# Performance work log

Measured on AMD Instinct MI355X. Metric: run time of the kernel, lower is better.

## Reference

```python
import jax, jax.numpy as jnp
import numpy as np

B, D, N = 2, 256, 8192   # batch, in_channels, sequence length
CI = 128                 # inter_channels
BN_EPS = 1e-5


def conv1x1(w, b, x):
    # w: (Cout, Cin), b: (Cout,), x: (B, Cin, N) -> (B, Cout, N)
    return jnp.einsum('oc,bcn->bon', w, x) + b[None, :, None]


def maxpool2(x):
    # MaxPool1d(kernel_size=2): (B, C, N) -> (B, C, N//2)
    b, c, n = x.shape
    return x.reshape(b, c, n // 2, 2).max(axis=-1)


def setup_inputs() -> dict:
    key = jax.random.key(0)
    ks = jax.random.split(key, 11)
    s_in = 1.0 / np.sqrt(D)
    s_ci = 1.0 / np.sqrt(CI)
    return {
        'f': jax.random.normal(ks[0], (B, D, N), dtype=jnp.float32),
        'g_w': jax.random.uniform(ks[1], (CI, D), jnp.float32, -s_in, s_in),
        'g_b': jax.random.uniform(ks[2], (CI,), jnp.float32, -s_in, s_in),
        'theta_w': jax.random.uniform(ks[3], (CI, D), jnp.float32, -s_in, s_in),
        'theta_b': jax.random.uniform(ks[4], (CI,), jnp.float32, -s_in, s_in),
        'phi_w': jax.random.uniform(ks[5], (CI, D), jnp.float32, -s_in, s_in),
        'phi_b': jax.random.uniform(ks[6], (CI,), jnp.float32, -s_in, s_in),
        'W_w': jax.random.uniform(ks[7], (D, CI), jnp.float32, -s_ci, s_ci),
        'W_b': jax.random.uniform(ks[8], (D,), jnp.float32, -s_ci, s_ci),
        'bn_gamma': jax.random.normal(ks[9], (D,), dtype=jnp.float32) * 0.1,
        'bn_beta': jax.random.normal(ks[10], (D,), dtype=jnp.float32) * 0.1,
    }


def reference(f, g_w, g_b, theta_w, theta_b, phi_w, phi_b, W_w, W_b, bn_gamma, bn_beta):
    # projections (1x1 convs); g and phi are sub-sampled by maxpool(2)
    g_f = maxpool2(conv1x1(g_w, g_b, f))          # (B, CI, N/2)
    theta_f = conv1x1(theta_w, theta_b, f)        # (B, CI, N)
    phi_f = maxpool2(conv1x1(phi_w, phi_b, f))    # (B, CI, N/2)

    # affinity: theta^T @ phi, softmax over keys (no scale, as in source)
    A = jnp.einsum('bcn,bcm->bnm', theta_f, phi_f)     # (B, N, N/2)
    A = jax.nn.softmax(A, axis=-1)
    y = jnp.einsum('bnm,bcm->bcn', A, g_f)             # (B, CI, N)

    # W: 1x1 conv + BatchNorm1d (training-mode batch stats), residual
    Wy = conv1x1(W_w, W_b, y)                          # (B, D, N)
    mean = Wy.mean(axis=(0, 2), keepdims=True)
    var = Wy.var(axis=(0, 2), keepdims=True)           # biased, like torch BN
    Wy = (Wy - mean) * jax.lax.rsqrt(var + BN_EPS)
    Wy = Wy * bn_gamma[None, :, None] + bn_beta[None, :, None]
    return Wy + f
```

## Files before the change

### kernel.cpp

```cpp
#include <hip/hip_runtime.h>
#include <hip/hip_bf16.h>
#include <math.h>

#define B_ 2
#define D_ 256
#define N_ 8192
#define CI_ 128
#define M_ 4096
#define BN_EPS_ 1e-5f

#define OFF_WALL 0
#define OFF_THT  49152
#define OFF_PHT  (OFF_THT + 1048576)
#define OFF_GT   (OFF_PHT + 524288)
#define OFF_YP   (OFF_GT  + 524288)
#define OFF_ML   (OFF_YP  + 4194304)
#define OFF_Y    (OFF_ML  + 131072)
#define OFF_MEAN (OFF_Y + 2097152)
#define OFF_RSTD (OFF_MEAN + 256)

typedef __attribute__((ext_vector_type(8))) short bfrag;
typedef __attribute__((ext_vector_type(4))) float f4v;
typedef __attribute__((ext_vector_type(16))) float f16v;
typedef __attribute__((ext_vector_type(4))) short s4v;

__device__ inline unsigned short bf16rne(float x) {
    unsigned u = __float_as_uint(x);
    u += 0x7fff + ((u >> 16) & 1);
    return (unsigned short)(u >> 16);
}

__global__ __launch_bounds__(256) void wconv_kernel(
    const float* __restrict__ gw, const float* __restrict__ tw, const float* __restrict__ pw,
    short* __restrict__ wall)
{
    int idx = blockIdx.x * 256 + threadIdx.x;
    int which = idx >> 15;
    int rem = idx & 32767;
    const float* src = (which == 0) ? gw : (which == 1) ? tw : pw;
    wall[idx] = (short)bf16rne(src[rem]);
}

__global__ __launch_bounds__(256, 2) void proj_kernel(
    const float* __restrict__ f, const short* __restrict__ wall,
    const float* __restrict__ tb, const float* __restrict__ gb, const float* __restrict__ pb,
    short* __restrict__ th_t, short* __restrict__ g_t, short* __restrict__ ph_t)
{
    __shared__ short sF[32 * 72];

    const int tid = threadIdx.x;
    const int wave = tid >> 6, lane = tid & 63;
    const int lq = lane & 15, quad = lane >> 4;
    const int b = blockIdx.y;
    const int n0 = blockIdx.x * 32;

    const float* fb = f + (size_t)b * D_ * N_;

    f4v acc[6][2];
#pragma unroll
    for (int ct = 0; ct < 6; ct++)
#pragma unroll
        for (int nf = 0; nf < 2; nf++) acc[ct][nf] = (f4v){0.f, 0.f, 0.f, 0.f};

    const int sn = tid & 31;
    const int sgrp = tid >> 5;

    for (int kc = 0; kc < D_; kc += 64) {
        __syncthreads();
#pragma unroll
        for (int jj = 0; jj < 4; jj++) {
            int dd = kc + sgrp * 8 + 2 * jj;
            float v0 = fb[(size_t)dd * N_ + n0 + sn];
            float v1 = fb[(size_t)(dd + 1) * N_ + n0 + sn];
            unsigned pk = (unsigned)bf16rne(v0) | ((unsigned)bf16rne(v1) << 16);
            *(unsigned*)&sF[sn * 72 + sgrp * 8 + 2 * jj] = pk;
        }
        __syncthreads();

        bfrag afr[6][2], bfr[2][2];
#pragma unroll
        for (int ks = 0; ks < 2; ks++) {
#pragma unroll
            for (int nf = 0; nf < 2; nf++)
                bfr[nf][ks] = *(const bfrag*)&sF[(nf * 16 + lq) * 72 + ks * 32 + quad * 8];
#pragma unroll
            for (int ct = 0; ct < 6; ct++)
                afr[ct][ks] = *(const bfrag*)&wall[(wave * 96 + ct * 16 + lq) * 256 + kc + ks * 32 + quad * 8];
        }
#pragma unroll
        for (int ks = 0; ks < 2; ks++)
#pragma unroll
            for (int ct = 0; ct < 6; ct++) {
                acc[ct][0] = __builtin_amdgcn_mfma_f32_16x16x32_bf16(afr[ct][ks], bfr[0][ks], acc[ct][0], 0, 0, 0);
                acc[ct][1] = __builtin_amdgcn_mfma_f32_16x16x32_bf16(afr[ct][ks], bfr[1][ks], acc[ct][1], 0, 0, 0);
            }
    }

#pragma unroll
    for (int ct = 0; ct < 6; ct++) {
        const int cf = wave * 6 + ct;
#pragma unroll
        for (int nf = 0; nf < 2; nf++) {
            f4v v = acc[ct][nf];
            const int n = n0 + nf * 16 + lq;
            if (cf < 8) {
                const int cb = cf * 16 + quad * 4;
                float pl[4];
#pragma unroll
                for (int r = 0; r < 4; r++) {
                    float o = __shfl_xor(v[r], 1);
                    pl[r] = fmaxf(v[r], o) + gb[cb + r];
                }
                if (!(lq & 1)) {
                    const int m = n >> 1;
#pragma unroll
                    for (int r = 0; r < 4; r++)
                        g_t[((size_t)b * CI_ + cb + r) * M_ + m] = (short)bf16rne(pl[r]);
                }
            } else if (cf < 16) {
                const int cb = (cf - 8) * 16 + quad * 4;
                s4v o;
#pragma unroll
                for (int r = 0; r < 4; r++) o[r] = (short)bf16rne(v[r] + tb[cb + r]);
                *(s4v*)&th_t[((size_t)b * N_ + n) * CI_ + cb] = o;
            } else {
                const int cb = (cf - 16) * 16 + quad * 4;
                float pl[4];
#pragma unroll
                for (int r = 0; r < 4; r++) {
                    float o = __shfl_xor(v[r], 1);
                    pl[r] = fmaxf(v[r], o) + pb[cb + r];
                }
                if (!(lq & 1)) {
                    const int m = n >> 1;
                    s4v o;
#pragma unroll
                    for (int r = 0; r < 4; r++) o[r] = (short)bf16rne(pl[r]);
                    *(s4v*)&ph_t[((size_t)b * M_ + m) * CI_ + cb] = o;
                }
            }
        }
    }
}

__global__ __launch_bounds__(256, 2) void attn_kernel(
    const short* __restrict__ th_p, const short* __restrict__ ph_p,
    const short* __restrict__ g_p, short* __restrict__ yp, float* __restrict__ ml)
{
    __shared__ short sPh[64 * 136];
    __shared__ short sG [128 * 72];
    __shared__ short sP [4 * 32 * 88];

    const int tid = threadIdx.x;
    const int wave = tid >> 6, lane = tid & 63;
    const int l = lane & 31, h = lane >> 5;
    const int b = blockIdx.y, split = blockIdx.z;
    const int q0 = blockIdx.x * 128;
    const int qg = q0 + wave * 32 + l;

    const short* thr = th_p + ((size_t)b * N_ + qg) * CI_;
    bfrag tf[8];
#pragma unroll
    for (int s = 0; s < 8; s++)
        tf[s] = *(const bfrag*)&thr[s * 16 + h * 8];

    f16v yacc[4];
#pragma unroll
    for (int ct = 0; ct < 4; ct++)
#pragma unroll
        for (int r = 0; r < 16; r++) yacc[ct][r] = 0.f;
    float mI = -INFINITY, lI = 0.f;

    const short* phg = ph_p + (size_t)b * M_ * CI_;
    const short* gg  = g_p + (size_t)b * CI_ * M_;
    short* sPw = &sP[wave * (32 * 88)];

    const int k0 = split * 1024;
    for (int kc = k0; kc < k0 + 1024; kc += 64) {
        __syncthreads();
#pragma unroll
        for (int p = 0; p < 4; p++) {
            int idx = p * 256 + tid;
            int r = idx >> 4, u = idx & 15;
            *(float4*)&sPh[r * 136 + u * 8] = *(const float4*)&phg[(size_t)(kc + r) * 128 + u * 8];
        }
#pragma unroll
        for (int p = 0; p < 4; p++) {
            int idx = p * 256 + tid;
            int r = idx >> 3, u = idx & 7;
            *(float4*)&sG[r * 72 + u * 8] = *(const float4*)&gg[(size_t)r * M_ + kc + u * 8];
        }
        __syncthreads();

        f16v sv[2];
#pragma unroll
        for (int kt = 0; kt < 2; kt++) {
            f16v a;
#pragma unroll
            for (int r = 0; r < 16; r++) a[r] = 0.f;
#pragma unroll
            for (int s = 0; s < 8; s++) {
                bfrag pa = *(const bfrag*)&sPh[(kt * 32 + l) * 136 + s * 16 + h * 8];
                a = __builtin_amdgcn_mfma_f32_32x32x16_bf16(pa, tf[s], a, 0, 0, 0);
            }
            sv[kt] = a;
        }

        float mx = sv[0][0];
#pragma unroll
        for (int kt = 0; kt < 2; kt++)
#pragma unroll
            for (int r = 0; r < 16; r++) mx = fmaxf(mx, sv[kt][r]);
        mx = fmaxf(mx, __shfl_xor(mx, 32));
        float mnew = fmaxf(mI, mx);
        float al = __expf(mI - mnew);
        float ps = 0.f;
#pragma unroll
        for (int kt = 0; kt < 2; kt++)
#pragma unroll
            for (int i = 0; i < 8; i++) {
                int r = 2 * i;
                float p0 = __expf(sv[kt][r] - mnew);
                float p1 = __expf(sv[kt][r + 1] - mnew);
                ps += p0 + p1;
                unsigned pk = (unsigned)bf16rne(p0) | ((unsigned)bf16rne(p1) << 16);
                int key = kt * 32 + (r & 3) + 8 * (r >> 2) + 4 * h;
                *(unsigned*)&sPw[l * 88 + key] = pk;
            }
        ps += __shfl_xor(ps, 32);
        lI = lI * al + ps;
        mI = mnew;

#pragma unroll
        for (int ct = 0; ct < 4; ct++)
#pragma unroll
            for (int r = 0; r < 16; r++) yacc[ct][r] *= al;

        bfrag pf[4];
#pragma unroll
        for (int s = 0; s < 4; s++)
            pf[s] = *(const bfrag*)&sPw[l * 88 + s * 16 + h * 8];
#pragma unroll
        for (int ct = 0; ct < 4; ct++)
#pragma unroll
            for (int s = 0; s < 4; s++) {
                bfrag ga = *(const bfrag*)&sG[(ct * 32 + l) * 72 + s * 16 + h * 8];
                yacc[ct] = __builtin_amdgcn_mfma_f32_32x32x16_bf16(ga, pf[s], yacc[ct], 0, 0, 0);
            }
    }

    short* yb = yp + (((size_t)split * B_ + b) * CI_) * N_;
#pragma unroll
    for (int ct = 0; ct < 4; ct++)
#pragma unroll
        for (int r = 0; r < 16; r++) {
            int c = ct * 32 + (r & 3) + 8 * (r >> 2) + 4 * h;
            yb[(size_t)c * N_ + qg] = (short)bf16rne(yacc[ct][r]);
        }
    if (h == 0) {
        float* mlb = ml + ((split * B_ + b) * 2) * N_;
        mlb[qg] = mI;
        mlb[N_ + qg] = lI;
    }
}

__global__ __launch_bounds__(256) void merge_kernel(
    const short* __restrict__ yp, const float* __restrict__ ml, float* __restrict__ y)
{
    int idx = blockIdx.x * 256 + threadIdx.x;
    int b = blockIdx.y;
    int e = idx * 4;
    int c = e >> 13;
    int n0 = e & (N_ - 1);

    float4 mv[4], lv[4];
#pragma unroll
    for (int s = 0; s < 4; s++) {
        const float* mlb = ml + ((s * B_ + b) * 2) * N_;
        mv[s] = *(const float4*)&mlb[n0];
        lv[s] = *(const float4*)&mlb[N_ + n0];
    }
    float ms[4] = {-INFINITY, -INFINITY, -INFINITY, -INFINITY};
#pragma unroll
    for (int s = 0; s < 4; s++) {
        ms[0] = fmaxf(ms[0], mv[s].x); ms[1] = fmaxf(ms[1], mv[s].y);
        ms[2] = fmaxf(ms[2], mv[s].z); ms[3] = fmaxf(ms[3], mv[s].w);
    }
    float num[4] = {0.f, 0.f, 0.f, 0.f}, den[4] = {0.f, 0.f, 0.f, 0.f};
#pragma unroll
    for (int s = 0; s < 4; s++) {
        s4v yv4 = *(const s4v*)&yp[(((size_t)s * B_ + b) * CI_ + c) * N_ + n0];
        float es[4];
        es[0] = __expf(mv[s].x - ms[0]); es[1] = __expf(mv[s].y - ms[1]);
        es[2] = __expf(mv[s].z - ms[2]); es[3] = __expf(mv[s].w - ms[3]);
        den[0] += lv[s].x * es[0]; den[1] += lv[s].y * es[1];
        den[2] += lv[s].z * es[2]; den[3] += lv[s].w * es[3];
#pragma unroll
        for (int j = 0; j < 4; j++) {
            float yv = __uint_as_float((unsigned)(unsigned short)yv4[j] << 16);
            num[j] += yv * es[j];
        }
    }
    float4 o;
    o.x = num[0] / den[0]; o.y = num[1] / den[1];
    o.z = num[2] / den[2]; o.w = num[3] / den[3];
    *(float4*)&y[((size_t)b * CI_ + c) * N_ + n0] = o;
}

__global__ __launch_bounds__(256) void wy_kernel(
    const float* __restrict__ y, const float* __restrict__ Ww,
    const float* __restrict__ Wb, float* __restrict__ out)
{
    int n = blockIdx.x * 256 + threadIdx.x;
    int d0 = blockIdx.y * 32;
    int b = blockIdx.z;
    const float* ypb = y + (size_t)b * CI_ * N_ + n;
    float acc[32];
#pragma unroll
    for (int dd = 0; dd < 32; dd++) acc[dd] = 0.f;
#pragma unroll 4
    for (int c = 0; c < CI_; c++) {
        float yv = ypb[(size_t)c * N_];
#pragma unroll
        for (int dd = 0; dd < 32; dd++)
            acc[dd] = fmaf(Ww[(d0 + dd) * CI_ + c], yv, acc[dd]);
    }
    float* op = out + (size_t)b * D_ * N_ + (size_t)d0 * N_ + n;
#pragma unroll
    for (int dd = 0; dd < 32; dd++) op[(size_t)dd * N_] = acc[dd] + Wb[d0 + dd];
}

__global__ __launch_bounds__(256) void stats_kernel(
    const float* __restrict__ wy, float* __restrict__ mean, float* __restrict__ rstd)
{
    __shared__ float ssum[256], ssq[256];
    int d = blockIdx.x;
    int tid = threadIdx.x;
    float s = 0.f, sq = 0.f;
    for (int b = 0; b < B_; b++) {
        const float* p = wy + (size_t)b * D_ * N_ + (size_t)d * N_;
        for (int i = tid; i < N_; i += 256) {
            float v = p[i];
            s += v;
            sq = fmaf(v, v, sq);
        }
    }
    ssum[tid] = s; ssq[tid] = sq;
    __syncthreads();
    for (int st = 128; st > 0; st >>= 1) {
        if (tid < st) { ssum[tid] += ssum[tid + st]; ssq[tid] += ssq[tid + st]; }
        __syncthreads();
    }
    if (tid == 0) {
        float inv = 1.0f / (float)(B_ * N_);
        float mn = ssum[0] * inv;
        float var = ssq[0] * inv - mn * mn;
        mean[d] = mn;
        rstd[d] = rsqrtf(var + BN_EPS_);
    }
}

__global__ __launch_bounds__(256) void bn_res_kernel(
    float* __restrict__ out, const float* __restrict__ f,
    const float* __restrict__ mean, const float* __restrict__ rstd,
    const float* __restrict__ gamma, const float* __restrict__ beta)
{
    int i = blockIdx.x * 256 + threadIdx.x;
    size_t e = (size_t)i * 4;
    int d = (int)((e >> 13) & 255);
    float4 wy = ((const float4*)out)[i];
    float4 ff = ((const float4*)f)[i];
    float sc = rstd[d] * gamma[d];
    float mn = mean[d];
    float bt = beta[d];
    float4 r;
    r.x = (wy.x - mn) * sc + bt + ff.x;
    r.y = (wy.y - mn) * sc + bt + ff.y;
    r.z = (wy.z - mn) * sc + bt + ff.z;
    r.w = (wy.w - mn) * sc + bt + ff.w;
    ((float4*)out)[i] = r;
}

extern "C" void kernel_launch(void* const* d_in, const int* in_sizes, int n_in,
                              void* d_out, int out_size, void* d_ws, size_t ws_size,
                              hipStream_t stream)
{
    const float* f   = (const float*)d_in[0];
    const float* g_w = (const float*)d_in[1];
    const float* g_b = (const float*)d_in[2];
    const float* t_w = (const float*)d_in[3];
    const float* t_b = (const float*)d_in[4];
    const float* p_w = (const float*)d_in[5];
    const float* p_b = (const float*)d_in[6];
    const float* W_w = (const float*)d_in[7];
    const float* W_b = (const float*)d_in[8];
    const float* gam = (const float*)d_in[9];
    const float* bet = (const float*)d_in[10];
    float* out = (float*)d_out;
    float* ws = (float*)d_ws;

    short* wall = (short*)(ws + OFF_WALL);
    short* th_t = (short*)(ws + OFF_THT);
    short* ph_t = (short*)(ws + OFF_PHT);
    short* g_t  = (short*)(ws + OFF_GT);
    short* ypart = (short*)(ws + OFF_YP);
    float* mlp = ws + OFF_ML;
    float* yws = ws + OFF_Y;
    float* mnp = ws + OFF_MEAN;
    float* rsp = ws + OFF_RSTD;

    wconv_kernel<<<384, 256, 0, stream>>>(g_w, t_w, p_w, wall);
    proj_kernel<<<dim3(N_ / 32, B_), 256, 0, stream>>>(f, wall, t_b, g_b, p_b,
                                                       th_t, g_t, ph_t);
    attn_kernel<<<dim3(N_ / 128, B_, 4), 256, 0, stream>>>(th_t, ph_t, g_t, ypart, mlp);
    merge_kernel<<<dim3(CI_ * N_ / 4 / 256, B_), 256, 0, stream>>>(ypart, mlp, yws);
    wy_kernel<<<dim3(N_ / 256, D_ / 32, B_), 256, 0, stream>>>(yws, W_w, W_b, out);
    stats_kernel<<<D_, 256, 0, stream>>>(out, mnp, rsp);
    bn_res_kernel<<<(B_ * D_ * N_ / 4) / 256, 256, 0, stream>>>(out, f, mnp, rsp, gam, bet);
}
```

Before: 224.9 us.

## Fuse split merge into bf16 MFMA W-projection and pass P fragments via shuffles

The separate merge and fp32 scalar W-conv kernels are replaced by one kernel. It combines the four split-K partial outputs in registers and runs the W projection with bf16 MFMA, using a W_w copy converted to bf16 in the weight-conversion kernel. This removes the fp32 y round trip through global memory and the scalar FMA GEMM, at the cost of bf16 rounding on y and W. In attention, the softmax probabilities are rearranged into MFMA operand layout with cross-half-wave shuffles instead of going through LDS. That frees shared memory and raises the occupancy hint to 3 blocks per CU, which may pressure registers.

```diff
diff --git a/kernel.cpp b/kernel.cpp
--- a/kernel.cpp
+++ b/kernel.cpp
@@ -10,13 +10,12 @@
 #define BN_EPS_ 1e-5f
 
 #define OFF_WALL 0
-#define OFF_THT  49152
+#define OFF_THT  65536
 #define OFF_PHT  (OFF_THT + 1048576)
 #define OFF_GT   (OFF_PHT + 524288)
 #define OFF_YP   (OFF_GT  + 524288)
 #define OFF_ML   (OFF_YP  + 4194304)
-#define OFF_Y    (OFF_ML  + 131072)
-#define OFF_MEAN (OFF_Y + 2097152)
+#define OFF_MEAN (OFF_ML + 131072)
 #define OFF_RSTD (OFF_MEAN + 256)
 
 typedef __attribute__((ext_vector_type(8))) short bfrag;
@@ -32,12 +31,12 @@
 
 __global__ __launch_bounds__(256) void wconv_kernel(
     const float* __restrict__ gw, const float* __restrict__ tw, const float* __restrict__ pw,
-    short* __restrict__ wall)
+    const float* __restrict__ Ww, short* __restrict__ wall)
 {
     int idx = blockIdx.x * 256 + threadIdx.x;
     int which = idx >> 15;
     int rem = idx & 32767;
-    const float* src = (which == 0) ? gw : (which == 1) ? tw : pw;
+    const float* src = (which == 0) ? gw : (which == 1) ? tw : (which == 2) ? pw : Ww;
     wall[idx] = (short)bf16rne(src[rem]);
 }
 
@@ -143,13 +142,12 @@
     }
 }
 
-__global__ __launch_bounds__(256, 2) void attn_kernel(
+__global__ __launch_bounds__(256, 3) void attn_kernel(
     const short* __restrict__ th_p, const short* __restrict__ ph_p,
     const short* __restrict__ g_p, short* __restrict__ yp, float* __restrict__ ml)
 {
     __shared__ short sPh[64 * 136];
     __shared__ short sG [128 * 72];
-    __shared__ short sP [4 * 32 * 88];
 
     const int tid = threadIdx.x;
     const int wave = tid >> 6, lane = tid & 63;
@@ -173,7 +171,6 @@
 
     const short* phg = ph_p + (size_t)b * M_ * CI_;
     const short* gg  = g_p + (size_t)b * CI_ * M_;
-    short* sPw = &sP[wave * (32 * 88)];
 
     const int k0 = split * 1024;
     for (int kc = k0; kc < k0 + 1024; kc += 64) {
@@ -215,6 +212,7 @@
         float mnew = fmaxf(mI, mx);
         float al = __expf(mI - mnew);
         float ps = 0.f;
+        unsigned pu[16];
 #pragma unroll
         for (int kt = 0; kt < 2; kt++)
 #pragma unroll
@@ -223,23 +221,36 @@
                 float p0 = __expf(sv[kt][r] - mnew);
                 float p1 = __expf(sv[kt][r + 1] - mnew);
                 ps += p0 + p1;
-                unsigned pk = (unsigned)bf16rne(p0) | ((unsigned)bf16rne(p1) << 16);
-                int key = kt * 32 + (r & 3) + 8 * (r >> 2) + 4 * h;
-                *(unsigned*)&sPw[l * 88 + key] = pk;
+                pu[kt * 8 + (i >> 1) * 2 + (i & 1)] =
+                    (unsigned)bf16rne(p0) | ((unsigned)bf16rne(p1) << 16);
             }
         ps += __shfl_xor(ps, 32);
         lI = lI * al + ps;
         mI = mnew;
 
+        bfrag pf[4];
+#pragma unroll
+        for (int s = 0; s < 4; s++) {
+            const int kt = s >> 1;
+            const int bo = (2 * s + h) & 3;
+            const int bx = (2 * s + (h ^ 1)) & 3;
+            unsigned O0 = pu[kt * 8 + bo * 2 + 0];
+            unsigned O1 = pu[kt * 8 + bo * 2 + 1];
+            unsigned X0 = (unsigned)__shfl_xor((int)pu[kt * 8 + bx * 2 + 0], 32);
+            unsigned X1 = (unsigned)__shfl_xor((int)pu[kt * 8 + bx * 2 + 1], 32);
+            union { unsigned u[4]; bfrag v; } t;
+            t.u[0] = h ? X0 : O0;
+            t.u[1] = h ? X1 : O1;
+            t.u[2] = h ? O0 : X0;
+            t.u[3] = h ? O1 : X1;
+            pf[s] = t.v;
+        }
+
 #pragma unroll
         for (int ct = 0; ct < 4; ct++)
 #pragma unroll
             for (int r = 0; r < 16; r++) yacc[ct][r] *= al;
 
-        bfrag pf[4];
-#pragma unroll
-        for (int s = 0; s < 4; s++)
-            pf[s] = *(const bfrag*)&sPw[l * 88 + s * 16 + h * 8];
 #pragma unroll
         for (int ct = 0; ct < 4; ct++)
 #pragma unroll
@@ -264,70 +275,70 @@
     }
 }
 
-__global__ __launch_bounds__(256) void merge_kernel(
-    const short* __restrict__ yp, const float* __restrict__ ml, float* __restrict__ y)
-{
-    int idx = blockIdx.x * 256 + threadIdx.x;
-    int b = blockIdx.y;
-    int e = idx * 4;
-    int c = e >> 13;
-    int n0 = e & (N_ - 1);
-
-    float4 mv[4], lv[4];
-#pragma unroll
-    for (int s = 0; s < 4; s++) {
-        const float* mlb = ml + ((s * B_ + b) * 2) * N_;
-        mv[s] = *(const float4*)&mlb[n0];
-        lv[s] = *(const float4*)&mlb[N_ + n0];
-    }
-    float ms[4] = {-INFINITY, -INFINITY, -INFINITY, -INFINITY};
-#pragma unroll
-    for (int s = 0; s < 4; s++) {
-        ms[0] = fmaxf(ms[0], mv[s].x); ms[1] = fmaxf(ms[1], mv[s].y);
-        ms[2] = fmaxf(ms[2], mv[s].z); ms[3] = fmaxf(ms[3], mv[s].w);
-    }
-    float num[4] = {0.f, 0.f, 0.f, 0.f}, den[4] = {0.f, 0.f, 0.f, 0.f};
-#pragma unroll
-    for (int s = 0; s < 4; s++) {
-        s4v yv4 = *(const s4v*)&yp[(((size_t)s * B_ + b) * CI_ + c) * N_ + n0];
-        float es[4];
-        es[0] = __expf(mv[s].x - ms[0]); es[1] = __expf(mv[s].y - ms[1]);
-        es[2] = __expf(mv[s].z - ms[2]); es[3] = __expf(mv[s].w - ms[3]);
-        den[0] += lv[s].x * es[0]; den[1] += lv[s].y * es[1];
-        den[2] += lv[s].z * es[2]; den[3] += lv[s].w * es[3];
-#pragma unroll
-        for (int j = 0; j < 4; j++) {
-            float yv = __uint_as_float((unsigned)(unsigned short)yv4[j] << 16);
-            num[j] += yv * es[j];
-        }
-    }
-    float4 o;
-    o.x = num[0] / den[0]; o.y = num[1] / den[1];
-    o.z = num[2] / den[2]; o.w = num[3] / den[3];
-    *(float4*)&y[((size_t)b * CI_ + c) * N_ + n0] = o;
-}
-
-__global__ __launch_bounds__(256) void wy_kernel(
-    const float* __restrict__ y, const float* __restrict__ Ww,
-    const float* __restrict__ Wb, float* __restrict__ out)
-{
-    int n = blockIdx.x * 256 + threadIdx.x;
-    int d0 = blockIdx.y * 32;
-    int b = blockIdx.z;
-    const float* ypb = y + (size_t)b * CI_ * N_ + n;
-    float acc[32];
-#pragma unroll
-    for (int dd = 0; dd < 32; dd++) acc[dd] = 0.f;
-#pragma unroll 4
-    for (int c = 0; c < CI_; c++) {
-        float yv = ypb[(size_t)c * N_];
-#pragma unroll
-        for (int dd = 0; dd < 32; dd++)
-            acc[dd] = fmaf(Ww[(d0 + dd) * CI_ + c], yv, acc[dd]);
-    }
-    float* op = out + (size_t)b * D_ * N_ + (size_t)d0 * N_ + n;
-#pragma unroll
-    for (int dd = 0; dd < 32; dd++) op[(size_t)dd * N_] = acc[dd] + Wb[d0 + dd];
+__global__ __launch_bounds__(256) void wy_merge_kernel(
+    const short* __restrict__ yp, const float* __restrict__ ml,
+    const short* __restrict__ wall2, const float* __restrict__ Wb,
+    float* __restrict__ out)
+{
+    const int tid = threadIdx.x;
+    const int wave = tid >> 6, lane = tid & 63;
+    const int l = lane & 31, h = lane >> 5;
+    const int b = blockIdx.y;
+    const int n = blockIdx.x * 32 + l;
+
+    float m[4], lv[4];
+#pragma unroll
+    for (int sp = 0; sp < 4; sp++) {
+        const float* mlb = ml + ((sp * B_ + b) * 2) * N_;
+        m[sp] = mlb[n];
+        lv[sp] = mlb[N_ + n];
+    }
+    float mmax = fmaxf(fmaxf(m[0], m[1]), fmaxf(m[2], m[3]));
+    float e[4], den = 0.f;
+#pragma unroll
+    for (int sp = 0; sp < 4; sp++) { e[sp] = __expf(m[sp] - mmax); den += lv[sp] * e[sp]; }
+    float inv = 1.0f / den;
+#pragma unroll
+    for (int sp = 0; sp < 4; sp++) e[sp] *= inv;
+
+    const unsigned short* ypu = (const unsigned short*)yp;
+    bfrag by[8];
+#pragma unroll
+    for (int s = 0; s < 8; s++) {
+#pragma unroll
+        for (int j = 0; j < 8; j++) {
+            const int c = s * 16 + h * 8 + j;
+            float a = 0.f;
+#pragma unroll
+            for (int sp = 0; sp < 4; sp++) {
+                unsigned short v = ypu[(((size_t)sp * B_ + b) * CI_ + c) * N_ + n];
+                a = fmaf(e[sp], __uint_as_float((unsigned)v << 16), a);
+            }
+            by[s][j] = (short)bf16rne(a);
+        }
+    }
+
+    f16v acc[2];
+#pragma unroll
+    for (int rt = 0; rt < 2; rt++)
+#pragma unroll
+        for (int r = 0; r < 16; r++) acc[rt][r] = 0.f;
+
+#pragma unroll
+    for (int s = 0; s < 8; s++)
+#pragma unroll
+        for (int rt = 0; rt < 2; rt++) {
+            bfrag aw = *(const bfrag*)&wall2[((wave * 2 + rt) * 32 + l) * 128 + s * 16 + h * 8];
+            acc[rt] = __builtin_amdgcn_mfma_f32_32x32x16_bf16(aw, by[s], acc[rt], 0, 0, 0);
+        }
+
+#pragma unroll
+    for (int rt = 0; rt < 2; rt++)
+#pragma unroll
+        for (int r = 0; r < 16; r++) {
+            const int d = (wave * 2 + rt) * 32 + (r & 3) + 8 * (r >> 2) + 4 * h;
+            out[((size_t)b * D_ + d) * N_ + n] = acc[rt][r] + Wb[d];
+        }
 }
 
 __global__ __launch_bounds__(256) void stats_kernel(
@@ -399,22 +410,21 @@
     float* out = (float*)d_out;
     float* ws = (float*)d_ws;
 
-    short* wall = (short*)(ws + OFF_WALL);
+    short* wall  = (short*)(ws + OFF_WALL);
+    short* wall2 = wall + 3 * 32768;
     short* th_t = (short*)(ws + OFF_THT);
     short* ph_t = (short*)(ws + OFF_PHT);
     short* g_t  = (short*)(ws + OFF_GT);
     short* ypart = (short*)(ws + OFF_YP);
     float* mlp = ws + OFF_ML;
-    float* yws = ws + OFF_Y;
     float* mnp = ws + OFF_MEAN;
     float* rsp = ws + OFF_RSTD;
 
-    wconv_kernel<<<384, 256, 0, stream>>>(g_w, t_w, p_w, wall);
+    wconv_kernel<<<512, 256, 0, stream>>>(g_w, t_w, p_w, W_w, wall);
     proj_kernel<<<dim3(N_ / 32, B_), 256, 0, stream>>>(f, wall, t_b, g_b, p_b,
                                                        th_t, g_t, ph_t);
     attn_kernel<<<dim3(N_ / 128, B_, 4), 256, 0, stream>>>(th_t, ph_t, g_t, ypart, mlp);
-    merge_kernel<<<dim3(CI_ * N_ / 4 / 256, B_), 256, 0, stream>>>(ypart, mlp, yws);
-    wy_kernel<<<dim3(N_ / 256, D_ / 32, B_), 256, 0, stream>>>(yws, W_w, W_b, out);
+    wy_merge_kernel<<<dim3(N_ / 32, B_), 256, 0, stream>>>(ypart, mlp, wall2, W_b, out);
     stats_kernel<<<D_, 256, 0, stream>>>(out, mnp, rsp);
     bn_res_kernel<<<(B_ * D_ * N_ / 4) / 256, 256, 0, stream>>>(out, f, mnp, rsp, gam, bet);
 }
```

Result: slower. 243.8 us (+8.4%).
